# Optimization experiments

Measured on AMD Instinct MI355X. Metric: run time of the kernel, lower is better.

The kernel has to match this reference:

```python
import jax, jax.numpy as jnp
import numpy as np

N_SLOTS = 64
DECAY = 0.999
B, S, H, M = 4, 4096, 2048, 128


def _l2norm(t, eps=1e-12):
    return t / jnp.maximum(jnp.linalg.norm(t, axis=-1, keepdims=True), eps)


def setup_inputs() -> dict:
    key = jax.random.key(0)
    ks = jax.random.split(key, 6)
    return {
        "x": jax.random.normal(ks[0], (B, S, H), dtype=jnp.float32),
        "W_query": jax.random.normal(ks[1], (M, H), dtype=jnp.float32) * 0.02,
        "W_key": jax.random.normal(ks[2], (M, H), dtype=jnp.float32) * 0.02,
        "W_value": jax.random.normal(ks[3], (M, H), dtype=jnp.float32) * 0.02,
        "W_out": jax.random.normal(ks[4], (H, M), dtype=jnp.float32) * 0.02,
        "W_gate_w": jax.random.normal(ks[5], (1, H), dtype=jnp.float32) * 0.02,
        "W_gate_b": jnp.full((1,), -2.0, dtype=jnp.float32),
        "log_beta": jnp.full((1,), np.log(8.0), dtype=jnp.float32),
        "chunk_size": 64,
    }


def reference(x, W_query, W_key, W_value, W_out, W_gate_w, W_gate_b, log_beta, chunk_size):
    b, s, h = x.shape
    m = W_query.shape[0]
    dt = x.dtype

    q = x @ W_query.T                      # (b, s, m)
    k = _l2norm(x @ W_key.T)               # (b, s, m)
    v = _l2norm(x @ W_value.T)             # (b, s, m)
    gate = jax.nn.sigmoid(x @ W_gate_w.T + W_gate_b)  # (b, s, 1)
    beta = jnp.exp(log_beta).reshape(())

    nc = s // chunk_size
    decay_c = jnp.asarray(DECAY, dt) ** chunk_size

    def chunkify(t):
        # (b, s, d) -> (nc, b, chunk, d)
        return jnp.moveaxis(t.reshape(b, nc, chunk_size, -1), 1, 0)

    qc, kc, vc = chunkify(q), chunkify(k), chunkify(v)
    wc = chunkify(gate)[..., 0]            # (nc, b, chunk)

    K0 = jnp.zeros((N_SLOTS, m), dt)
    V0 = jnp.zeros((N_SLOTS, m), dt)
    s0 = jnp.zeros((N_SLOTS,), dt)
    ptr0 = jnp.asarray(0, jnp.int32)

    def step(carry, inp):
        K_mem, V_mem, mem_strength, ptr = carry
        qch, kch, vch, wch = inp           # (b,c,m) x3, (b,c)
        # --- read: softmax retrieval over active slots ---
        slot_mask = (mem_strength > 1e-8).astype(dt)           # (n_slots,)
        scores = jnp.einsum("bcm,nm->bcn", qch, K_mem) * beta
        scores = scores + (1.0 - slot_mask) * -1e9
        attn = jax.nn.softmax(scores, axis=-1)
        r = jnp.einsum("bcn,nm->bcm", attn, V_mem)
        r = jnp.where(mem_strength.sum() < 1e-8, jnp.zeros_like(r), r)
        # --- write: gated aggregation into one slot ---
        w_sum = jnp.maximum(wch.sum(), 1e-8)
        k_agg = _l2norm((kch * wch[..., None]).sum((0, 1)) / w_sum)
        v_agg = _l2norm((vch * wch[..., None]).sum((0, 1)) / w_sum)
        write_str = wch.mean()
        mem_strength = mem_strength * decay_c
        slot = ptr % N_SLOTS
        K_mem = K_mem.at[slot].set(k_agg)
        V_mem = V_mem.at[slot].set(v_agg)
        mem_strength = mem_strength.at[slot].set(write_str)
        return (K_mem, V_mem, mem_strength, ptr + 1), (r, write_str)

    _, (rs, wss) = jax.lax.scan(step, (K0, V0, s0, ptr0), (qc, kc, vc, wc))

    retrieved = jnp.moveaxis(rs, 0, 1).reshape(b, s, m)
    out = retrieved @ W_out.T              # (b, s, h)
    # clamp output norm to 10
    onorm = jnp.maximum(jnp.linalg.norm(out, axis=-1, keepdims=True), 1e-6)
    out = out * jnp.minimum(10.0 / onorm, 1.0)
    mean_ws = jnp.mean(wss)
    return out, mean_ws
```

## Files before the change

### kernel.cpp

```cpp
#include <hip/hip_runtime.h>
#include <math.h>
#include <stdint.h>

#define NTOK 16384
#define SEQ  4096
#define HD   2048
#define MD   128
#define NCH  64
#define CHK  64

typedef __attribute__((ext_vector_type(8))) _Float16 half8;
typedef __attribute__((ext_vector_type(4))) float floatx4;

__device__ __forceinline__ void gload_lds16(const void* g, void* l) {
    __builtin_amdgcn_global_load_lds(
        (const __attribute__((address_space(1))) unsigned int*)(uintptr_t)g,
        (__attribute__((address_space(3))) unsigned int*)(uintptr_t)l,
        16, 0, 0);
}

__global__ __launch_bounds__(256) void convert_w_kernel(
    const float* __restrict__ Wq, const float* __restrict__ Wk,
    const float* __restrict__ Wv, const float* __restrict__ Wo,
    _Float16* __restrict__ Wcath, _Float16* __restrict__ Woh)
{
    int i = blockIdx.x * 256 + threadIdx.x;
    if (i < 384 * HD) {
        int r = i >> 11;
        float val;
        if (r < 128)      val = Wq[i];
        else if (r < 256) val = Wk[i - 128 * HD];
        else              val = Wv[i - 256 * HD];
        Wcath[i] = (_Float16)val;
    } else {
        int j = i - 384 * HD;
        Woh[j] = (_Float16)Wo[j];
    }
}

__global__ __launch_bounds__(128) void gmat_kernel(
    const float* __restrict__ Wo, float* __restrict__ G)
{
    __shared__ float col[HD];
    int a = blockIdx.x;
    int b = threadIdx.x;
    for (int j = b; j < HD; j += 128) col[j] = Wo[(size_t)j * MD + a];
    __syncthreads();
    float s = 0.f;
    for (int j = 0; j < HD; ++j) s = fmaf(col[j], Wo[(size_t)j * MD + b], s);
    G[a * MD + b] = s;
}

__global__ __launch_bounds__(256) void convert_x_gate_kernel(
    const float* __restrict__ x, const float* __restrict__ Wgw,
    const float* __restrict__ gb,
    _Float16* __restrict__ xh, float* __restrict__ wg)
{
    int row = blockIdx.x;
    int tid = threadIdx.x;
    const float* xr = x + (size_t)row * HD;
    float4 a = *(const float4*)&xr[tid * 8];
    float4 b = *(const float4*)&xr[tid * 8 + 4];
    float4 wa = *(const float4*)&Wgw[tid * 8];
    float4 wb = *(const float4*)&Wgw[tid * 8 + 4];
    float p = a.x * wa.x + a.y * wa.y + a.z * wa.z + a.w * wa.w
            + b.x * wb.x + b.y * wb.y + b.z * wb.z + b.w * wb.w;

    half8 h;
    h[0] = (_Float16)a.x; h[1] = (_Float16)a.y;
    h[2] = (_Float16)a.z; h[3] = (_Float16)a.w;
    h[4] = (_Float16)b.x; h[5] = (_Float16)b.y;
    h[6] = (_Float16)b.z; h[7] = (_Float16)b.w;
    *(half8*)&xh[(size_t)row * HD + tid * 8] = h;

    int wave = tid >> 6, lane = tid & 63;
    #pragma unroll
    for (int off = 32; off > 0; off >>= 1) p += __shfl_xor(p, off);
    __shared__ float red[4];
    if (lane == 0) red[wave] = p;
    __syncthreads();
    if (tid == 0) {
        float t = red[0] + red[1] + red[2] + red[3] + gb[0];
        wg[row] = 1.f / (1.f + expf(-t));
    }
}

__device__ __forceinline__ void mfma_loop(
    const _Float16* __restrict__ A, int lda,
    const _Float16* __restrict__ B, int ldb,
    int row0, int col0, int K,
    _Float16* As, _Float16* Bs, floatx4 acc[4][4])
{
    const int tid  = threadIdx.x;
    const int wave = tid >> 6, lane = tid & 63;
    const int wm = wave & 1, wn = wave >> 1;
    const int seg_r = lane >> 2;
    const int chunk = lane & 3;

    for (int k0 = 0; k0 < K; k0 += 32) {
        #pragma unroll
        for (int rnd = 0; rnd < 2; ++rnd) {
            int s = wave + 4 * rnd;
            int r = s * 16 + seg_r;
            gload_lds16(A + (size_t)(row0 + r) * lda + k0 + chunk * 8,
                        As + s * 512);
            gload_lds16(B + (size_t)(col0 + r) * ldb + k0 + chunk * 8,
                        Bs + s * 512);
        }
        __syncthreads();
        half8 af[4], bf[4];
        #pragma unroll
        for (int i = 0; i < 4; ++i) {
            af[i] = *(const half8*)&As[(wm * 64 + i * 16 + (lane & 15)) * 32 + (lane >> 4) * 8];
            bf[i] = *(const half8*)&Bs[(wn * 64 + i * 16 + (lane & 15)) * 32 + (lane >> 4) * 8];
        }
        #pragma unroll
        for (int i = 0; i < 4; ++i)
            #pragma unroll
            for (int j = 0; j < 4; ++j)
                acc[i][j] = __builtin_amdgcn_mfma_f32_16x16x32_f16(
                    af[i], bf[j], acc[i][j], 0, 0, 0);
        __syncthreads();
    }
}

__global__ __launch_bounds__(256) void gemm_proj_mfma(
    const _Float16* __restrict__ xh, const _Float16* __restrict__ Wcath,
    float* __restrict__ q, float* __restrict__ k, float* __restrict__ v)
{
    __shared__ _Float16 As[4096], Bs[4096];
    floatx4 acc[4][4];
    #pragma unroll
    for (int i = 0; i < 4; ++i)
        #pragma unroll
        for (int j = 0; j < 4; ++j) acc[i][j] = (floatx4){0.f, 0.f, 0.f, 0.f};

    int row0 = blockIdx.x * 128;
    int col0 = blockIdx.y * 128;
    mfma_loop(xh, HD, Wcath, HD, row0, col0, HD, As, Bs, acc);

    float* dst = (blockIdx.y == 0) ? q : ((blockIdx.y == 1) ? k : v);
    int wave = threadIdx.x >> 6, lane = threadIdx.x & 63;
    int wm = wave & 1, wn = wave >> 1;
    #pragma unroll
    for (int i = 0; i < 4; ++i) {
        int m = row0 + wm * 64 + i * 16 + (lane >> 4) * 4;
        #pragma unroll
        for (int j = 0; j < 4; ++j) {
            int c = wn * 64 + j * 16 + (lane & 15);
            #pragma unroll
            for (int r = 0; r < 4; ++r)
                dst[(size_t)(m + r) * MD + c] = acc[i][j][r];
        }
    }
}

__global__ __launch_bounds__(256) void normsig_kernel(
    float* __restrict__ k, float* __restrict__ v)
{
    int wave = threadIdx.x >> 6, lane = threadIdx.x & 63;
    int row = blockIdx.x * 4 + wave;
    size_t base = (size_t)row * MD + lane * 2;
    float2 k2 = *reinterpret_cast<float2*>(&k[base]);
    float2 v2 = *reinterpret_cast<float2*>(&v[base]);
    float ks = k2.x * k2.x + k2.y * k2.y;
    float vs = v2.x * v2.x + v2.y * v2.y;
    #pragma unroll
    for (int off = 32; off > 0; off >>= 1) {
        ks += __shfl_xor(ks, off);
        vs += __shfl_xor(vs, off);
    }
    float ki = 1.f / fmaxf(sqrtf(ks), 1e-12f);
    float vi = 1.f / fmaxf(sqrtf(vs), 1e-12f);
    k2.x *= ki; k2.y *= ki; v2.x *= vi; v2.y *= vi;
    *reinterpret_cast<float2*>(&k[base]) = k2;
    *reinterpret_cast<float2*>(&v[base]) = v2;
}

__global__ __launch_bounds__(256) void agg_kernel(
    const float* __restrict__ kn, const float* __restrict__ vn,
    const float* __restrict__ w,
    float* __restrict__ kaT, float* __restrict__ vagg, float* __restrict__ wstr)
{
    int t   = blockIdx.x;
    int tid = threadIdx.x;
    int d = tid & 127, h = tid >> 7;
    __shared__ float s_k[128], s_v[128], s_red[256];

    float ka = 0.f, va = 0.f;
    for (int jj = 0; jj < 128; ++jj) {
        int j = h * 128 + jj;
        int b = j >> 6, c = j & 63;
        int row = b * SEQ + t * CHK + c;
        float wv = w[row];
        ka = fmaf(wv, kn[(size_t)row * MD + d], ka);
        va = fmaf(wv, vn[(size_t)row * MD + d], va);
    }
    if (h == 1) { s_k[d] = ka; s_v[d] = va; }
    { int b = tid >> 6, c = tid & 63; s_red[tid] = w[b * SEQ + t * CHK + c]; }
    __syncthreads();
    if (h == 0) { ka += s_k[d]; va += s_v[d]; }
    for (int s = 128; s > 0; s >>= 1) {
        if (tid < s) s_red[tid] += s_red[tid + s];
        __syncthreads();
    }
    float wsum = s_red[0];
    float winv = 1.f / fmaxf(wsum, 1e-8f);
    float ku = ka * winv, vu = va * winv;
    __syncthreads();
    if (h == 0) s_red[d] = ku * ku;
    __syncthreads();
    for (int s = 64; s > 0; s >>= 1) {
        if (tid < s) s_red[tid] += s_red[tid + s];
        __syncthreads();
    }
    float kinv = 1.f / fmaxf(sqrtf(s_red[0]), 1e-12f);
    __syncthreads();
    if (h == 0) s_red[d] = vu * vu;
    __syncthreads();
    for (int s = 64; s > 0; s >>= 1) {
        if (tid < s) s_red[tid] += s_red[tid + s];
        __syncthreads();
    }
    float vinv = 1.f / fmaxf(sqrtf(s_red[0]), 1e-12f);
    if (h == 0) {
        kaT[d * NCH + t]  = ku * kinv;
        vagg[t * MD + d]  = vu * vinv;
        if (d == 0) wstr[t] = wsum * (1.f / 256.f);
    }
}

__global__ __launch_bounds__(64) void meanws_kernel(
    const float* __restrict__ wstr, float* __restrict__ outp)
{
    int lane = threadIdx.x;
    float v = wstr[lane];
    #pragma unroll
    for (int off = 32; off > 0; off >>= 1) v += __shfl_xor(v, off);
    if (lane == 0) outp[0] = v * (1.f / 64.f);
}

__global__ __launch_bounds__(256) void attn_kernel(
    const float* __restrict__ q, const float* __restrict__ kaT,
    const float* __restrict__ vagg, const float* __restrict__ G,
    const float* __restrict__ logbeta, _Float16* __restrict__ rsh16)
{
    __shared__ float qs[4][128];
    __shared__ float attn_s[4][64];
    __shared__ float rsh[4][128];
    int wave = threadIdx.x >> 6, lane = threadIdx.x & 63;
    int row = blockIdx.x * 4 + wave;
    int t = (row & (SEQ - 1)) >> 6;
    float beta = expf(logbeta[0]);

    qs[wave][lane]      = q[(size_t)row * MD + lane];
    qs[wave][lane + 64] = q[(size_t)row * MD + 64 + lane];
    __syncthreads();

    float sc = -INFINITY;
    if (lane < t) {
        sc = 0.f;
        for (int d = 0; d < 128; ++d)
            sc = fmaf(qs[wave][d], kaT[d * NCH + lane], sc);
        sc *= beta;
    }
    float mx = sc;
    #pragma unroll
    for (int off = 32; off > 0; off >>= 1) mx = fmaxf(mx, __shfl_xor(mx, off));
    float e = (lane < t) ? expf(sc - mx) : 0.f;
    float ssum = e;
    #pragma unroll
    for (int off = 32; off > 0; off >>= 1) ssum += __shfl_xor(ssum, off);
    float attn = (t > 0) ? (e / ssum) : 0.f;
    attn_s[wave][lane] = attn;
    __syncthreads();

    float r0 = 0.f, r1 = 0.f;
    for (int n = 0; n < t; ++n) {
        float a = attn_s[wave][n];
        r0 = fmaf(a, vagg[n * MD + lane], r0);
        r1 = fmaf(a, vagg[n * MD + 64 + lane], r1);
    }
    rsh[wave][lane]      = r0;
    rsh[wave][lane + 64] = r1;
    __syncthreads();

    float t0 = 0.f, t1 = 0.f;
    for (int b = 0; b < 128; ++b) {
        float rb = rsh[wave][b];
        t0 = fmaf(G[b * MD + lane], rb, t0);
        t1 = fmaf(G[b * MD + 64 + lane], rb, t1);
    }
    float quad = r0 * t0 + r1 * t1;
    #pragma unroll
    for (int off = 32; off > 0; off >>= 1) quad += __shfl_xor(quad, off);
    float nrm = fmaxf(sqrtf(fmaxf(quad, 0.f)), 1e-6f);
    float scl = fminf(10.f / nrm, 1.f);
    rsh16[(size_t)row * MD + lane]      = (_Float16)(r0 * scl);
    rsh16[(size_t)row * MD + 64 + lane] = (_Float16)(r1 * scl);
}

__global__ __launch_bounds__(256) void gemm_out_mfma(
    const _Float16* __restrict__ rsh16, const _Float16* __restrict__ Woh,
    float* __restrict__ C)
{
    __shared__ _Float16 As[4096], Bs[4096];
    floatx4 acc[4][4];
    #pragma unroll
    for (int i = 0; i < 4; ++i)
        #pragma unroll
        for (int j = 0; j < 4; ++j) acc[i][j] = (floatx4){0.f, 0.f, 0.f, 0.f};

    int row0 = blockIdx.x * 128;
    int col0 = blockIdx.y * 128;
    mfma_loop(rsh16, MD, Woh, MD, row0, col0, MD, As, Bs, acc);

    int wave = threadIdx.x >> 6, lane = threadIdx.x & 63;
    int wm = wave & 1, wn = wave >> 1;
    #pragma unroll
    for (int i = 0; i < 4; ++i) {
        int m = row0 + wm * 64 + i * 16 + (lane >> 4) * 4;
        #pragma unroll
        for (int j = 0; j < 4; ++j) {
            int c = col0 + wn * 64 + j * 16 + (lane & 15);
            #pragma unroll
            for (int r = 0; r < 4; ++r)
                C[(size_t)(m + r) * HD + c] = acc[i][j][r];
        }
    }
}

extern "C" void kernel_launch(void* const* d_in, const int* in_sizes, int n_in,
                              void* d_out, int out_size, void* d_ws, size_t ws_size,
                              hipStream_t stream)
{
    const float* x   = (const float*)d_in[0];
    const float* Wq  = (const float*)d_in[1];
    const float* Wk  = (const float*)d_in[2];
    const float* Wv  = (const float*)d_in[3];
    const float* Wo  = (const float*)d_in[4];
    const float* Wgw = (const float*)d_in[5];
    const float* Wgb = (const float*)d_in[6];
    const float* lb  = (const float*)d_in[7];
    float* out = (float*)d_out;

    _Float16* xh = (_Float16*)d_ws;
    float* q    = (float*)(xh + (size_t)NTOK * HD);
    float* kn   = q + (size_t)NTOK * MD;
    float* vn   = kn + (size_t)NTOK * MD;
    float* wg   = vn + (size_t)NTOK * MD;
    float* kaT  = wg + NTOK;
    float* vagg = kaT + MD * NCH;
    float* wstr = vagg + NCH * MD;
    float* G    = wstr + 64;
    _Float16* Wcath = (_Float16*)(G + MD * MD);
    _Float16* Woh   = Wcath + 384 * HD;
    _Float16* rsh16 = Woh + HD * MD;

    convert_w_kernel<<<dim3(4096), dim3(256), 0, stream>>>(Wq, Wk, Wv, Wo, Wcath, Woh);
    gmat_kernel<<<dim3(128), dim3(128), 0, stream>>>(Wo, G);
    convert_x_gate_kernel<<<dim3(NTOK), dim3(256), 0, stream>>>(x, Wgw, Wgb, xh, wg);
    gemm_proj_mfma<<<dim3(NTOK / 128, 3), dim3(256), 0, stream>>>(xh, Wcath, q, kn, vn);
    normsig_kernel<<<dim3(NTOK / 4), dim3(256), 0, stream>>>(kn, vn);
    agg_kernel<<<dim3(NCH), dim3(256), 0, stream>>>(kn, vn, wg, kaT, vagg, wstr);
    meanws_kernel<<<dim3(1), dim3(64), 0, stream>>>(wstr, out + (size_t)NTOK * HD);
    attn_kernel<<<dim3(NTOK / 4), dim3(256), 0, stream>>>(q, kaT, vagg, G, lb, rsh16);
    gemm_out_mfma<<<dim3(NTOK / 128, HD / 128), dim3(256), 0, stream>>>(rsh16, Woh, out);
}
```

Before: 427.6 us.

## Fuse x fp16 conversion and gate into projection GEMM; split chunk aggregation

The projection GEMM now reads fp32 x directly, converts it to fp16 in registers and stores it into LDS, and the y==0 blocks also compute the gate dot product and sigmoid. This removes the separate conversion kernel and the round trip of the fp16 copy of x through memory. The catch is that x is read three times (once per column block), and the A-tile load becomes a synchronous register path instead of an async global-to-LDS copy. Separately, the per-chunk aggregation is split into a 256-block partial kernel and a small combine kernel to raise parallelism.

```diff
diff --git a/kernel.cpp b/kernel.cpp
--- a/kernel.cpp
+++ b/kernel.cpp
@@ -51,62 +51,68 @@
     G[a * MD + b] = s;
 }
 
-__global__ __launch_bounds__(256) void convert_x_gate_kernel(
-    const float* __restrict__ x, const float* __restrict__ Wgw,
-    const float* __restrict__ gb,
-    _Float16* __restrict__ xh, float* __restrict__ wg)
-{
-    int row = blockIdx.x;
-    int tid = threadIdx.x;
-    const float* xr = x + (size_t)row * HD;
-    float4 a = *(const float4*)&xr[tid * 8];
-    float4 b = *(const float4*)&xr[tid * 8 + 4];
-    float4 wa = *(const float4*)&Wgw[tid * 8];
-    float4 wb = *(const float4*)&Wgw[tid * 8 + 4];
-    float p = a.x * wa.x + a.y * wa.y + a.z * wa.z + a.w * wa.w
-            + b.x * wb.x + b.y * wb.y + b.z * wb.z + b.w * wb.w;
-
-    half8 h;
-    h[0] = (_Float16)a.x; h[1] = (_Float16)a.y;
-    h[2] = (_Float16)a.z; h[3] = (_Float16)a.w;
-    h[4] = (_Float16)b.x; h[5] = (_Float16)b.y;
-    h[6] = (_Float16)b.z; h[7] = (_Float16)b.w;
-    *(half8*)&xh[(size_t)row * HD + tid * 8] = h;
-
-    int wave = tid >> 6, lane = tid & 63;
-    #pragma unroll
-    for (int off = 32; off > 0; off >>= 1) p += __shfl_xor(p, off);
-    __shared__ float red[4];
-    if (lane == 0) red[wave] = p;
-    __syncthreads();
-    if (tid == 0) {
-        float t = red[0] + red[1] + red[2] + red[3] + gb[0];
-        wg[row] = 1.f / (1.f + expf(-t));
-    }
-}
-
-__device__ __forceinline__ void mfma_loop(
-    const _Float16* __restrict__ A, int lda,
-    const _Float16* __restrict__ B, int ldb,
-    int row0, int col0, int K,
-    _Float16* As, _Float16* Bs, floatx4 acc[4][4])
-{
+__global__ __launch_bounds__(256) void gemm_proj_mfma(
+    const float* __restrict__ x, const _Float16* __restrict__ Wcath,
+    const float* __restrict__ Wgw, const float* __restrict__ gb,
+    float* __restrict__ q, float* __restrict__ k, float* __restrict__ v,
+    float* __restrict__ wg)
+{
+    __shared__ _Float16 As[4096], Bs[4096];
+    floatx4 acc[4][4];
+    #pragma unroll
+    for (int i = 0; i < 4; ++i)
+        #pragma unroll
+        for (int j = 0; j < 4; ++j) acc[i][j] = (floatx4){0.f, 0.f, 0.f, 0.f};
+
     const int tid  = threadIdx.x;
     const int wave = tid >> 6, lane = tid & 63;
     const int wm = wave & 1, wn = wave >> 1;
     const int seg_r = lane >> 2;
     const int chunk = lane & 3;
-
-    for (int k0 = 0; k0 < K; k0 += 32) {
+    const int arow  = tid >> 1;
+    const int ahalf = tid & 1;
+    const int row0 = blockIdx.x * 128;
+    const int col0 = blockIdx.y * 128;
+    const bool do_gate = (blockIdx.y == 0);
+
+    float gacc = 0.f;
+
+    for (int k0 = 0; k0 < HD; k0 += 32) {
         #pragma unroll
         for (int rnd = 0; rnd < 2; ++rnd) {
             int s = wave + 4 * rnd;
             int r = s * 16 + seg_r;
-            gload_lds16(A + (size_t)(row0 + r) * lda + k0 + chunk * 8,
-                        As + s * 512);
-            gload_lds16(B + (size_t)(col0 + r) * ldb + k0 + chunk * 8,
+            gload_lds16(Wcath + (size_t)(col0 + r) * HD + k0 + chunk * 8,
                         Bs + s * 512);
         }
+        const float* ap = x + (size_t)(row0 + arow) * HD + k0 + ahalf * 16;
+        float4 a0 = *(const float4*)(ap);
+        float4 a1 = *(const float4*)(ap + 4);
+        float4 a2 = *(const float4*)(ap + 8);
+        float4 a3 = *(const float4*)(ap + 12);
+        if (do_gate) {
+            const float* wp = Wgw + k0 + ahalf * 16;
+            float4 w0 = *(const float4*)(wp);
+            float4 w1 = *(const float4*)(wp + 4);
+            float4 w2 = *(const float4*)(wp + 8);
+            float4 w3 = *(const float4*)(wp + 12);
+            gacc += a0.x * w0.x + a0.y * w0.y + a0.z * w0.z + a0.w * w0.w
+                  + a1.x * w1.x + a1.y * w1.y + a1.z * w1.z + a1.w * w1.w
+                  + a2.x * w2.x + a2.y * w2.y + a2.z * w2.z + a2.w * w2.w
+                  + a3.x * w3.x + a3.y * w3.y + a3.z * w3.z + a3.w * w3.w;
+        }
+        half8 h0, h1;
+        h0[0] = (_Float16)a0.x; h0[1] = (_Float16)a0.y;
+        h0[2] = (_Float16)a0.z; h0[3] = (_Float16)a0.w;
+        h0[4] = (_Float16)a1.x; h0[5] = (_Float16)a1.y;
+        h0[6] = (_Float16)a1.z; h0[7] = (_Float16)a1.w;
+        h1[0] = (_Float16)a2.x; h1[1] = (_Float16)a2.y;
+        h1[2] = (_Float16)a2.z; h1[3] = (_Float16)a2.w;
+        h1[4] = (_Float16)a3.x; h1[5] = (_Float16)a3.y;
+        h1[6] = (_Float16)a3.z; h1[7] = (_Float16)a3.w;
+        *(half8*)&As[arow * 32 + ahalf * 16]     = h0;
+        *(half8*)&As[arow * 32 + ahalf * 16 + 8] = h1;
+
         __syncthreads();
         half8 af[4], bf[4];
         #pragma unroll
@@ -122,26 +128,16 @@
                     af[i], bf[j], acc[i][j], 0, 0, 0);
         __syncthreads();
     }
-}
-
-__global__ __launch_bounds__(256) void gemm_proj_mfma(
-    const _Float16* __restrict__ xh, const _Float16* __restrict__ Wcath,
-    float* __restrict__ q, float* __restrict__ k, float* __restrict__ v)
-{
-    __shared__ _Float16 As[4096], Bs[4096];
-    floatx4 acc[4][4];
-    #pragma unroll
-    for (int i = 0; i < 4; ++i)
-        #pragma unroll
-        for (int j = 0; j < 4; ++j) acc[i][j] = (floatx4){0.f, 0.f, 0.f, 0.f};
-
-    int row0 = blockIdx.x * 128;
-    int col0 = blockIdx.y * 128;
-    mfma_loop(xh, HD, Wcath, HD, row0, col0, HD, As, Bs, acc);
+
+    if (do_gate) {
+        float g2 = gacc + __shfl_xor(gacc, 1);
+        if (ahalf == 0) {
+            int row = row0 + arow;
+            wg[row] = 1.f / (1.f + expf(-(g2 + gb[0])));
+        }
+    }
 
     float* dst = (blockIdx.y == 0) ? q : ((blockIdx.y == 1) ? k : v);
-    int wave = threadIdx.x >> 6, lane = threadIdx.x & 63;
-    int wm = wave & 1, wn = wave >> 1;
     #pragma unroll
     for (int i = 0; i < 4; ++i) {
         int m = row0 + wm * 64 + i * 16 + (lane >> 4) * 4;
@@ -177,57 +173,71 @@
     *reinterpret_cast<float2*>(&v[base]) = v2;
 }
 
-__global__ __launch_bounds__(256) void agg_kernel(
+__global__ __launch_bounds__(256) void agg_part_kernel(
     const float* __restrict__ kn, const float* __restrict__ vn,
     const float* __restrict__ w,
-    float* __restrict__ kaT, float* __restrict__ vagg, float* __restrict__ wstr)
-{
-    int t   = blockIdx.x;
+    float* __restrict__ kpart, float* __restrict__ vpart,
+    float* __restrict__ wpart)
+{
+    int t = blockIdx.x >> 2, b = blockIdx.x & 3;
     int tid = threadIdx.x;
     int d = tid & 127, h = tid >> 7;
-    __shared__ float s_k[128], s_v[128], s_red[256];
+    int base_row = b * SEQ + t * CHK;
 
     float ka = 0.f, va = 0.f;
-    for (int jj = 0; jj < 128; ++jj) {
-        int j = h * 128 + jj;
-        int b = j >> 6, c = j & 63;
-        int row = b * SEQ + t * CHK + c;
+    for (int c = h * 32; c < h * 32 + 32; ++c) {
+        int row = base_row + c;
         float wv = w[row];
         ka = fmaf(wv, kn[(size_t)row * MD + d], ka);
         va = fmaf(wv, vn[(size_t)row * MD + d], va);
     }
-    if (h == 1) { s_k[d] = ka; s_v[d] = va; }
-    { int b = tid >> 6, c = tid & 63; s_red[tid] = w[b * SEQ + t * CHK + c]; }
-    __syncthreads();
-    if (h == 0) { ka += s_k[d]; va += s_v[d]; }
-    for (int s = 128; s > 0; s >>= 1) {
-        if (tid < s) s_red[tid] += s_red[tid + s];
-        __syncthreads();
-    }
-    float wsum = s_red[0];
+    __shared__ float sk[128], sv[128];
+    if (h == 1) { sk[d] = ka; sv[d] = va; }
+    __syncthreads();
+    if (h == 0) {
+        kpart[(size_t)blockIdx.x * 128 + d] = ka + sk[d];
+        vpart[(size_t)blockIdx.x * 128 + d] = va + sv[d];
+    }
+    if (tid < 64) {
+        float wv = w[base_row + tid];
+        #pragma unroll
+        for (int off = 32; off > 0; off >>= 1) wv += __shfl_xor(wv, off);
+        if (tid == 0) wpart[blockIdx.x] = wv;
+    }
+}
+
+__global__ __launch_bounds__(128) void agg_combine_kernel(
+    const float* __restrict__ kpart, const float* __restrict__ vpart,
+    const float* __restrict__ wpart,
+    float* __restrict__ kaT, float* __restrict__ vagg, float* __restrict__ wstr)
+{
+    int t = blockIdx.x;
+    int d = threadIdx.x;
+    int wave = d >> 6, lane = d & 63;
+    float ku = 0.f, vu = 0.f;
+    #pragma unroll
+    for (int b = 0; b < 4; ++b) {
+        ku += kpart[(size_t)(t * 4 + b) * 128 + d];
+        vu += vpart[(size_t)(t * 4 + b) * 128 + d];
+    }
+    float wsum = wpart[t * 4] + wpart[t * 4 + 1] + wpart[t * 4 + 2] + wpart[t * 4 + 3];
     float winv = 1.f / fmaxf(wsum, 1e-8f);
-    float ku = ka * winv, vu = va * winv;
-    __syncthreads();
-    if (h == 0) s_red[d] = ku * ku;
-    __syncthreads();
-    for (int s = 64; s > 0; s >>= 1) {
-        if (tid < s) s_red[tid] += s_red[tid + s];
-        __syncthreads();
-    }
-    float kinv = 1.f / fmaxf(sqrtf(s_red[0]), 1e-12f);
-    __syncthreads();
-    if (h == 0) s_red[d] = vu * vu;
-    __syncthreads();
-    for (int s = 64; s > 0; s >>= 1) {
-        if (tid < s) s_red[tid] += s_red[tid + s];
-        __syncthreads();
-    }
-    float vinv = 1.f / fmaxf(sqrtf(s_red[0]), 1e-12f);
-    if (h == 0) {
-        kaT[d * NCH + t]  = ku * kinv;
-        vagg[t * MD + d]  = vu * vinv;
-        if (d == 0) wstr[t] = wsum * (1.f / 256.f);
-    }
+    ku *= winv; vu *= winv;
+
+    __shared__ float red[4];
+    float ks = ku * ku, vs = vu * vu;
+    #pragma unroll
+    for (int off = 32; off > 0; off >>= 1) {
+        ks += __shfl_xor(ks, off);
+        vs += __shfl_xor(vs, off);
+    }
+    if (lane == 0) { red[wave] = ks; red[2 + wave] = vs; }
+    __syncthreads();
+    float kinv = 1.f / fmaxf(sqrtf(red[0] + red[1]), 1e-12f);
+    float vinv = 1.f / fmaxf(sqrtf(red[2] + red[3]), 1e-12f);
+    kaT[d * NCH + t] = ku * kinv;
+    vagg[t * MD + d] = vu * vinv;
+    if (d == 0) wstr[t] = wsum * (1.f / 256.f);
 }
 
 __global__ __launch_bounds__(64) void meanws_kernel(
@@ -311,12 +321,40 @@
         #pragma unroll
         for (int j = 0; j < 4; ++j) acc[i][j] = (floatx4){0.f, 0.f, 0.f, 0.f};
 
-    int row0 = blockIdx.x * 128;
-    int col0 = blockIdx.y * 128;
-    mfma_loop(rsh16, MD, Woh, MD, row0, col0, MD, As, Bs, acc);
-
-    int wave = threadIdx.x >> 6, lane = threadIdx.x & 63;
-    int wm = wave & 1, wn = wave >> 1;
+    const int tid  = threadIdx.x;
+    const int wave = tid >> 6, lane = tid & 63;
+    const int wm = wave & 1, wn = wave >> 1;
+    const int seg_r = lane >> 2;
+    const int chunk = lane & 3;
+    const int row0 = blockIdx.x * 128;
+    const int col0 = blockIdx.y * 128;
+
+    for (int k0 = 0; k0 < MD; k0 += 32) {
+        #pragma unroll
+        for (int rnd = 0; rnd < 2; ++rnd) {
+            int s = wave + 4 * rnd;
+            int r = s * 16 + seg_r;
+            gload_lds16(rsh16 + (size_t)(row0 + r) * MD + k0 + chunk * 8,
+                        As + s * 512);
+            gload_lds16(Woh + (size_t)(col0 + r) * MD + k0 + chunk * 8,
+                        Bs + s * 512);
+        }
+        __syncthreads();
+        half8 af[4], bf[4];
+        #pragma unroll
+        for (int i = 0; i < 4; ++i) {
+            af[i] = *(const half8*)&As[(wm * 64 + i * 16 + (lane & 15)) * 32 + (lane >> 4) * 8];
+            bf[i] = *(const half8*)&Bs[(wn * 64 + i * 16 + (lane & 15)) * 32 + (lane >> 4) * 8];
+        }
+        #pragma unroll
+        for (int i = 0; i < 4; ++i)
+            #pragma unroll
+            for (int j = 0; j < 4; ++j)
+                acc[i][j] = __builtin_amdgcn_mfma_f32_16x16x32_f16(
+                    af[i], bf[j], acc[i][j], 0, 0, 0);
+        __syncthreads();
+    }
+
     #pragma unroll
     for (int i = 0; i < 4; ++i) {
         int m = row0 + wm * 64 + i * 16 + (lane >> 4) * 4;
@@ -344,8 +382,7 @@
     const float* lb  = (const float*)d_in[7];
     float* out = (float*)d_out;
 
-    _Float16* xh = (_Float16*)d_ws;
-    float* q    = (float*)(xh + (size_t)NTOK * HD);
+    float* q    = (float*)d_ws;
     float* kn   = q + (size_t)NTOK * MD;
     float* vn   = kn + (size_t)NTOK * MD;
     float* wg   = vn + (size_t)NTOK * MD;
@@ -353,16 +390,20 @@
     float* vagg = kaT + MD * NCH;
     float* wstr = vagg + NCH * MD;
     float* G    = wstr + 64;
-    _Float16* Wcath = (_Float16*)(G + MD * MD);
+    float* kpart = G + MD * MD;
+    float* vpart = kpart + 256 * 128;
+    float* wpart = vpart + 256 * 128;
+    _Float16* Wcath = (_Float16*)(wpart + 256);
     _Float16* Woh   = Wcath + 384 * HD;
     _Float16* rsh16 = Woh + HD * MD;
 
     convert_w_kernel<<<dim3(4096), dim3(256), 0, stream>>>(Wq, Wk, Wv, Wo, Wcath, Woh);
     gmat_kernel<<<dim3(128), dim3(128), 0, stream>>>(Wo, G);
-    convert_x_gate_kernel<<<dim3(NTOK), dim3(256), 0, stream>>>(x, Wgw, Wgb, xh, wg);
-    gemm_proj_mfma<<<dim3(NTOK / 128, 3), dim3(256), 0, stream>>>(xh, Wcath, q, kn, vn);
+    gemm_proj_mfma<<<dim3(NTOK / 128, 3), dim3(256), 0, stream>>>(
+        x, Wcath, Wgw, Wgb, q, kn, vn, wg);
     normsig_kernel<<<dim3(NTOK / 4), dim3(256), 0, stream>>>(kn, vn);
-    agg_kernel<<<dim3(NCH), dim3(256), 0, stream>>>(kn, vn, wg, kaT, vagg, wstr);
+    agg_part_kernel<<<dim3(256), dim3(256), 0, stream>>>(kn, vn, wg, kpart, vpart, wpart);
+    agg_combine_kernel<<<dim3(NCH), dim3(128), 0, stream>>>(kpart, vpart, wpart, kaT, vagg, wstr);
     meanws_kernel<<<dim3(1), dim3(64), 0, stream>>>(wstr, out + (size_t)NTOK * HD);
     attn_kernel<<<dim3(NTOK / 4), dim3(256), 0, stream>>>(q, kaT, vagg, G, lb, rsh16);
     gemm_out_mfma<<<dim3(NTOK / 128, HD / 128), dim3(256), 0, stream>>>(rsh16, Woh, out);
```

Measured after the change: 419.3 us. Within noise of the previous version (-1.9%).
